# Kernel optimization log

Hardware: AMD Instinct MI355X
Metric: run time of the kernel (lower is better)

The kernel has to match this reference:

```python
import jax, jax.numpy as jnp
from jax import lax
import numpy as np

B, T, H, L = 4096, 7, 512, 256
D = 2 * H  # bidirectional LSTM feature dim


def _lstm(x, wih, whh, bih, bhh, reverse):
    # x: [B, T, L]; torch gate order i, f, g, o
    b, hdim = x.shape[0], whh.shape[0]
    xs = jnp.swapaxes(x, 0, 1)  # [T, B, L]
    bias = bih + bhh

    def step(carry, xt):
        h, c = carry
        gates = xt @ wih + h @ whh + bias
        i, f, g, o = jnp.split(gates, 4, axis=-1)
        c = jax.nn.sigmoid(f) * c + jax.nn.sigmoid(i) * jnp.tanh(g)
        h = jax.nn.sigmoid(o) * jnp.tanh(c)
        return (h, c), h

    h0 = jnp.zeros((b, hdim), x.dtype)
    _, hs = lax.scan(step, (h0, h0), xs, reverse=reverse)
    return jnp.swapaxes(hs, 0, 1)  # [B, T, H]


def _att(enc, dec):
    # Sequential attention: keys/values start as enc and grow with each decoder output.
    keys = enc  # [B, T, D]
    outs = []
    for i in range(dec.shape[1]):  # fixed small T=7, Python loop is static
        q = dec[:, i, :]                                  # [B, D]
        scores = jnp.einsum('bd,btd->bt', q, keys)        # dot over features
        a = jax.nn.softmax(scores, axis=1)
        ctx = jnp.einsum('bt,btd->bd', a, keys)
        out = ctx + q
        outs.append(out)
        keys = jnp.concatenate([keys, out[:, None, :]], axis=1)
    return jnp.stack(outs, axis=1)  # [B, T, D]


def _deconv(x, w, b):
    # torch ConvTranspose2d (stride 1, pad 0) == full conv with flipped, in/out-swapped kernel
    kh, kw = w.shape[2], w.shape[3]
    w2 = jnp.transpose(w[:, :, ::-1, ::-1], (1, 0, 2, 3))  # [out, in, kh, kw]
    y = lax.conv_general_dilated(x, w2, (1, 1), ((kh - 1, kh - 1), (kw - 1, kw - 1)),
                                 dimension_numbers=('NCHW', 'OIHW', 'NCHW'))
    return y + b[None, :, None, None]


def setup_inputs() -> dict:
    key = jax.random.key(0)
    ks = jax.random.split(key, 12)
    p = lambda k, shape: jax.random.normal(k, shape, jnp.float32) * 0.02
    return {
        'lstm_enc': jax.random.normal(ks[0], (B, T, D), jnp.float32),
        'gaussian_noise': jax.random.normal(ks[1], (B, L), jnp.float32),
        'embedrep_w': p(ks[2], (L, L * T)), 'embedrep_b': jnp.zeros((L * T,), jnp.float32),
        'wih_f': p(ks[3], (L, 4 * H)), 'whh_f': p(ks[4], (H, 4 * H)),
        'bih_f': jnp.zeros((4 * H,), jnp.float32), 'bhh_f': jnp.zeros((4 * H,), jnp.float32),
        'wih_b': p(ks[5], (L, 4 * H)), 'whh_b': p(ks[6], (H, 4 * H)),
        'bih_b': jnp.zeros((4 * H,), jnp.float32), 'bhh_b': jnp.zeros((4 * H,), jnp.float32),
        'emb_w': p(ks[7], (D, 1024)), 'emb_b': jnp.zeros((1024,), jnp.float32),
        'dc3_w': p(ks[8], (64, 32, 1, 3)), 'dc3_b': jnp.zeros((32,), jnp.float32),
        'dc1_w': p(ks[9], (32, 16, 1, 5)), 'dc1_b': jnp.zeros((16,), jnp.float32),
        'dc2_w': p(ks[10], (16, 1, 3, 3)), 'dc2_b': jnp.zeros((1,), jnp.float32),
        'infer': 0,
    }


def reference(lstm_enc, gaussian_noise, embedrep_w, embedrep_b,
              wih_f, whh_f, bih_f, bhh_f, wih_b, whh_b, bih_b, bhh_b,
              emb_w, emb_b, dc3_w, dc3_b, dc1_w, dc1_b, dc2_w, dc2_b, infer):
    b = lstm_enc.shape[0]
    g1 = jax.nn.soft_sign(gaussian_noise @ embedrep_w + embedrep_b)   # [B, L*T]
    rep = g1.reshape(b, T, L)                                          # [B, 7, L]
    hf = _lstm(rep, wih_f, whh_f, bih_f, bhh_f, False)
    hb = _lstm(rep, wih_b, whh_b, bih_b, bhh_b, True)
    lstm1 = jnp.concatenate([hf, hb], axis=-1)                         # [B, 7, 2H]
    att_out = _att(lstm_enc, lstm1)                                    # [B, 7, 2H]
    emb = att_out @ emb_w + emb_b                                      # [B, 7, 1024]
    up = jax.nn.soft_sign(emb).reshape(b * T, 64, 1, 16)
    x = jax.nn.leaky_relu(_deconv(up, dc3_w, dc3_b))                   # [B*7, 32, 1, 18]
    x = jax.nn.leaky_relu(_deconv(x, dc1_w, dc1_b))                    # [B*7, 16, 1, 22]
    x = jax.nn.leaky_relu(_deconv(x, dc2_w, dc2_b))                    # [B*7, 1, 3, 24]
    x = jax.nn.softmax(x, axis=2)                                      # softmax over H dim (=3)
    out = x.reshape(b, T, 1, 3, 24)[:, :, -1, :, :]                    # [B, 7, 3, 24]
    return out
```

## Files before the change

kernel.cpp:

```cpp
#include <hip/hip_runtime.h>
#include <stdint.h>


typedef __attribute__((ext_vector_type(4))) float f32x4;
typedef __attribute__((ext_vector_type(8))) short bf16x8;
typedef __attribute__((ext_vector_type(4))) unsigned short us4;

__device__ __forceinline__ unsigned short f2b(float f) {
  union { float f; unsigned u; } x; x.f = f;
  unsigned r = x.u + 0x7FFFu + ((x.u >> 16) & 1u);
  return (unsigned short)(r >> 16);
}
__device__ __forceinline__ float b2f(unsigned short s) {
  union { unsigned u; float f; } x; x.u = ((unsigned)s) << 16; return x.f;
}
__device__ __forceinline__ float sigmoidf(float x) {
  return 1.f / (1.f + __expf(-x));
}
__device__ __forceinline__ float fast_tanh(float x) {
  x = fminf(15.f, fmaxf(-15.f, x));
  float e = __expf(2.f * x);
  return (e - 1.f) / (e + 1.f);
}

__device__ __forceinline__ void gl_lds16(const void* g, void* l) {
  auto gp = reinterpret_cast<const __attribute__((address_space(1))) unsigned int*>(
      reinterpret_cast<uintptr_t>(g));
  auto lp = reinterpret_cast<__attribute__((address_space(3))) unsigned int*>(
      reinterpret_cast<uintptr_t>(l));
  __builtin_amdgcn_global_load_lds(gp, lp, 16, 0, 0);
}


__device__ __forceinline__ void stage256x32(const unsigned short* src, int ld,
                                            unsigned short* hbase, int tid) {
  const int row_in = tid >> 2;
  const int gidx = tid & 3;
#pragma unroll
  for (int r = 0; r < 4; ++r) {
    int row = r * 64 + row_in;
    int gsrc = gidx ^ ((row >> 1) & 3);
    gl_lds16(src + (size_t)row * ld + gsrc * 8, hbase + r * 2048 + (tid >> 6) * 512);
  }
}

__device__ __forceinline__ void stage128x32(const unsigned short* src, int ld,
                                            unsigned short* hbase, int tid) {
  const int row_in = tid >> 2;
  const int gidx = tid & 3;
#pragma unroll
  for (int r = 0; r < 2; ++r) {
    int row = r * 64 + row_in;
    int gsrc = gidx ^ ((row >> 1) & 3);
    gl_lds16(src + (size_t)row * ld + gsrc * 8, hbase + r * 2048 + (tid >> 6) * 512);
  }
}

__device__ __forceinline__ void stage128x32_t128(const unsigned short* src, int ld,
                                                 unsigned short* hbase, int tid) {
  const int row_in = tid >> 2;
  const int gidx = tid & 3;
#pragma unroll
  for (int r = 0; r < 4; ++r) {
    int row = r * 32 + row_in;
    int gsrc = gidx ^ ((row >> 1) & 3);
    gl_lds16(src + (size_t)row * ld + gsrc * 8, hbase + r * 1024 + (tid >> 6) * 512);
  }
}

__device__ __forceinline__ bf16x8 lds_fragH(const unsigned short* hbase, int row, int lq) {
  return *(const bf16x8*)(hbase + row * 32 + (lq ^ (((row >> 1) & 3) << 3)));
}

__device__ __forceinline__ void tile_w128(const unsigned short* Ab, const unsigned short* Bb,
                                          int wm, int wn, int lane, f32x4 (&acc)[8][4]) {
  const int lr = lane & 15, lq = (lane >> 4) * 8;
  bf16x8 b[4];
#pragma unroll
  for (int n = 0; n < 4; ++n) b[n] = lds_fragH(Bb, wn * 64 + n * 16 + lr, lq);
  bf16x8 a[8];
#pragma unroll
  for (int i = 0; i < 8; ++i) a[i] = lds_fragH(Ab, wm * 128 + i * 16 + lr, lq);
  __builtin_amdgcn_s_setprio(1);
#pragma unroll
  for (int i = 0; i < 8; ++i)
#pragma unroll
    for (int n = 0; n < 4; ++n)
      acc[i][n] = __builtin_amdgcn_mfma_f32_16x16x32_bf16(a[i], b[n], acc[i][n], 0, 0, 0);
  __builtin_amdgcn_s_setprio(0);
}

#define DBUF_SYNC()                                   \
  asm volatile("s_waitcnt vmcnt(0)" ::: "memory");    \
  __builtin_amdgcn_s_barrier();                       \
  __builtin_amdgcn_sched_barrier(0);

__device__ __forceinline__ void stage128x64(const unsigned short* src, int ld,
                                            unsigned short* lds, int wv, int lane) {
#pragma unroll
  for (int r = 0; r < 4; ++r) {
    int row = r * 32 + wv * 8 + (lane >> 3);
    gl_lds16(src + (size_t)row * ld + (lane & 7) * 8, lds + (r * 32 + wv * 8) * 64);
  }
}
__device__ __forceinline__ void mfma_tile(const unsigned short* As, const unsigned short* Bs,
                                          int wm, int wn, int lane, f32x4 acc[4][4]) {
#pragma unroll
  for (int kk = 0; kk < 2; ++kk) {
    int ko = kk * 32 + (lane >> 4) * 8;
    bf16x8 a[4], b[4];
#pragma unroll
    for (int i = 0; i < 4; ++i)
      a[i] = *(const bf16x8*)(As + (size_t)(wm * 64 + i * 16 + (lane & 15)) * 64 + ko);
#pragma unroll
    for (int i = 0; i < 4; ++i)
      b[i] = *(const bf16x8*)(Bs + (size_t)(wn * 64 + i * 16 + (lane & 15)) * 64 + ko);
#pragma unroll
    for (int mi = 0; mi < 4; ++mi)
#pragma unroll
      for (int ni = 0; ni < 4; ++ni)
        acc[mi][ni] = __builtin_amdgcn_mfma_f32_16x16x32_bf16(a[mi], b[ni], acc[mi][ni], 0, 0, 0);
  }
}

__global__ __launch_bounds__(256) void pack_kernel(
    const float* __restrict__ noise, const float* __restrict__ erep_w,
    const float* __restrict__ emb_w,
    const float* __restrict__ wih_f, const float* __restrict__ whh_f,
    const float* __restrict__ bih_f, const float* __restrict__ bhh_f,
    const float* __restrict__ wih_b, const float* __restrict__ whh_b,
    const float* __restrict__ bih_b, const float* __restrict__ bhh_b,
    unsigned short* __restrict__ noiseb, unsigned short* __restrict__ erepT,
    unsigned short* __restrict__ embT, unsigned short* __restrict__ lstmW,
    float* __restrict__ lstmB) {
  const int N0 = 4096 * 256 / 4;
  const int N1 = 1792 * 256 / 4;
  const int N2 = 1024 * 1024 / 4;
  const int N3 = 2 * 2048 * 768 / 4;
  const int N4 = 2 * 2048 / 4;
  const int total = N0 + N1 + N2 + N3 + N4;
  for (int i = blockIdx.x * 256 + threadIdx.x; i < total; i += gridDim.x * 256) {
    int x = i;
    if (x < N0) {
      f32x4 v = ((const f32x4*)noise)[x];
      us4 o4;
#pragma unroll
      for (int e = 0; e < 4; ++e) o4[e] = f2b(v[e]);
      ((us4*)noiseb)[x] = o4;
      continue;
    }
    x -= N0;
    if (x < N1) {
      int n = x >> 6, k4 = (x & 63) * 4;
      us4 o4;
#pragma unroll
      for (int e = 0; e < 4; ++e) o4[e] = f2b(erep_w[(size_t)(k4 + e) * 1792 + n]);
      ((us4*)erepT)[x] = o4;
      continue;
    }
    x -= N1;
    if (x < N2) {
      int n = x >> 8, k4 = (x & 255) * 4;
      int o = (n & 63) * 16 + (n >> 6);
      us4 o4;
#pragma unroll
      for (int e = 0; e < 4; ++e) o4[e] = f2b(emb_w[(size_t)(k4 + e) * 1024 + o]);
      ((us4*)embT)[x] = o4;
      continue;
    }
    x -= N2;
    if (x < N3) {
      int dir = x / (2048 * 192);
      int r = x - dir * (2048 * 192);
      int npk = r / 192, k4 = (r - npk * 192) * 4;
      int blk = npk >> 6, g = (npk >> 4) & 3, u = npk & 15;
      int o = g * 512 + blk * 16 + u;
      const float* wih = dir ? wih_b : wih_f;
      const float* whh = dir ? whh_b : whh_f;
      us4 o4;
#pragma unroll
      for (int e = 0; e < 4; ++e) {
        int k = k4 + e;
        float v = (k < 256) ? wih[(size_t)k * 2048 + o] : whh[(size_t)(k - 256) * 2048 + o];
        o4[e] = f2b(v);
      }
      ((us4*)lstmW)[x] = o4;
      continue;
    }
    x -= N3;
    {
      int dir = x >> 9, npk4 = (x & 511) * 4;
      int blk = npk4 >> 6, g = (npk4 >> 4) & 3, u = npk4 & 15;
      int o = g * 512 + blk * 16 + u;
      const float* bi = dir ? bih_b : bih_f;
      const float* bh = dir ? bhh_b : bhh_f;
      f32x4 o4;
#pragma unroll
      for (int e = 0; e < 4; ++e) o4[e] = bi[o + e] + bh[o + e];
      ((f32x4*)lstmB)[x] = o4;
    }
  }
}

__global__ __launch_bounds__(256) void gemm_rep_kernel(
    const unsigned short* __restrict__ A, const unsigned short* __restrict__ Bt,
    const float* __restrict__ bias, unsigned short* __restrict__ rep_t) {
  __shared__ unsigned short As[128 * 64];
  __shared__ unsigned short Bs[128 * 64];
  const int lane = threadIdx.x & 63, wv = threadIdx.x >> 6;
  const int wm = wv >> 1, wn = wv & 1;
  const int m0 = blockIdx.y * 128, n0 = blockIdx.x * 128;
  f32x4 acc[4][4];
#pragma unroll
  for (int i = 0; i < 4; ++i)
#pragma unroll
    for (int j = 0; j < 4; ++j) acc[i][j] = (f32x4){0.f, 0.f, 0.f, 0.f};
  for (int k0 = 0; k0 < 256; k0 += 64) {
    stage128x64(A + (size_t)m0 * 256 + k0, 256, As, wv, lane);
    stage128x64(Bt + (size_t)n0 * 256 + k0, 256, Bs, wv, lane);
    __syncthreads();
    mfma_tile(As, Bs, wm, wn, lane, acc);
    __syncthreads();
  }
#pragma unroll
  for (int ni = 0; ni < 4; ++ni) {
    int n = n0 + wn * 64 + ni * 16 + (lane & 15);
    float bv = bias[n];
    int t = n >> 8, l = n & 255;
#pragma unroll
    for (int mi = 0; mi < 4; ++mi)
#pragma unroll
      for (int r = 0; r < 4; ++r) {
        int m = m0 + wm * 64 + mi * 16 + (lane >> 4) * 4 + r;
        float v = acc[mi][ni][r] + bv;
        v = v / (1.f + fabsf(v));
        rep_t[((size_t)t * 4096 + m) * 256 + l] = f2b(v);
      }
  }
}

__global__ __launch_bounds__(128, 2) void lstm_step_kernel(
    const unsigned short* __restrict__ rep_t, const unsigned short* __restrict__ Wp,
    const float* __restrict__ biasP, unsigned short* __restrict__ hbuf,
    unsigned short* __restrict__ cbuf, unsigned short* __restrict__ lstm1, int step) {
  __shared__ unsigned short Ar[2][4096];
  __shared__ unsigned short Br[2][4096];
  const int tid = threadIdx.x, lane = tid & 63, wv = tid >> 6;
  const int swz = (blockIdx.x & 7) * 128 + (blockIdx.x >> 3);
  const int dir = swz >> 9;
  const int rem = swz & 511;
  const int by = rem >> 4, bx = rem & 15;
  const int m0 = by * 128, n0 = bx * 128;
  const int t_proc = dir ? (6 - step) : step;
  const unsigned short* W = Wp + (size_t)dir * 2048 * 768;
  const unsigned short* hin = hbuf + ((size_t)(step & 1) * 2 + dir) * (4096 * 512);
  unsigned short* hout = hbuf + ((size_t)((step + 1) & 1) * 2 + dir) * (4096 * 512);
  unsigned short* cp = cbuf + (size_t)dir * (4096 * 512);
  const unsigned short* xsrc = rep_t + (size_t)t_proc * 4096 * 256;

  f32x4 acc[8][4];
#pragma unroll
  for (int i = 0; i < 8; ++i)
#pragma unroll
    for (int j = 0; j < 4; ++j) acc[i][j] = (f32x4){0.f, 0.f, 0.f, 0.f};

  auto asrc = [&](int tt) {
    return tt < 8 ? xsrc + (size_t)m0 * 256 + tt * 32
                  : hin + (size_t)m0 * 512 + (tt - 8) * 32;
  };
  auto ald = [&](int tt) { return tt < 8 ? 256 : 512; };

  stage128x32_t128(asrc(0), ald(0), Ar[0], tid);
  stage128x32_t128(W + (size_t)n0 * 768 + 0 * 32, 768, Br[0], tid);
  DBUF_SYNC()

#pragma unroll
  for (int t = 0; t < 24; ++t) {
    if (t + 1 < 24) {
      stage128x32_t128(asrc(t + 1), ald(t + 1), Ar[(t + 1) & 1], tid);
      stage128x32_t128(W + (size_t)n0 * 768 + (t + 1) * 32, 768, Br[(t + 1) & 1], tid);
    }
    tile_w128(Ar[t & 1], Br[t & 1], 0, wv, lane, acc);
    if (t + 1 < 24) { DBUF_SYNC() }
  }

  const int u = lane & 15;
  const int blk = (n0 + wv * 64) >> 6;
  const int j = blk * 16 + u;
  const float bz0 = biasP[dir * 2048 + blk * 64 + 0 * 16 + u];
  const float bz1 = biasP[dir * 2048 + blk * 64 + 1 * 16 + u];
  const float bz2 = biasP[dir * 2048 + blk * 64 + 2 * 16 + u];
  const float bz3 = biasP[dir * 2048 + blk * 64 + 3 * 16 + u];
#pragma unroll
  for (int mi = 0; mi < 8; ++mi)
#pragma unroll
    for (int r = 0; r < 4; ++r) {
      int row = m0 + mi * 16 + (lane >> 4) * 4 + r;
      float gi = acc[mi][0][r] + bz0;
      float gf = acc[mi][1][r] + bz1;
      float gg = acc[mi][2][r] + bz2;
      float go = acc[mi][3][r] + bz3;
      size_t ci = (size_t)row * 512 + j;
      float c = sigmoidf(gf) * b2f(cp[ci]) + sigmoidf(gi) * fast_tanh(gg);
      cp[ci] = f2b(c);
      float h = sigmoidf(go) * fast_tanh(c);
      unsigned short hb = f2b(h);
      hout[ci] = hb;
      lstm1[((size_t)row * 7 + t_proc) * 1024 + dir * 512 + j] = hb;
    }
}

__global__ __launch_bounds__(256) void att_fused3_kernel(
    const float* __restrict__ enc, const unsigned short* __restrict__ lstm1,
    unsigned short* __restrict__ att) {
  __shared__ unsigned short Qs[7 * 1032];
  __shared__ unsigned short Es[7 * 1032];
  __shared__ float P[8 * 256];
  __shared__ float sG[98];
  __shared__ float sC[7][14];
  __shared__ float sA[16];
  const int tid = threadIdx.x, lane = tid & 63, wv = tid >> 6;
  const int b = blockIdx.x;
  const float* Eb = enc + (size_t)b * 7168;
  const unsigned short* Qb = lstm1 + (size_t)b * 7168;

  if (tid < 98) ((float*)sC)[tid] = 0.f;

  const f32x4* Eb4 = (const f32x4*)Eb;
  const int d0 = tid * 4;
#pragma unroll
  for (int r = 0; r < 7; ++r) {
    f32x4 v = Eb4[r * 256 + tid];
    us4 hi;
#pragma unroll
    for (int e = 0; e < 4; ++e) hi[e] = f2b(v[e]);
    *(us4*)&Es[r * 1032 + d0] = hi;
    *(us4*)&Qs[r * 1032 + d0] = *(const us4*)(Qb + r * 1024 + d0);
  }
  asm volatile("s_waitcnt lgkmcnt(0)" ::: "memory");
  __builtin_amdgcn_sched_barrier(0);

  {
    const int rr = lane & 15;
    const int rowc = rr % 7;
    const int kbase = wv * 256 + (lane >> 4) * 8;
    f32x4 g1 = {0.f, 0.f, 0.f, 0.f}, g2 = {0.f, 0.f, 0.f, 0.f};
#pragma unroll
    for (int s = 0; s < 8; ++s) {
      const int k0 = kbase + s * 32;
      bf16x8 aq = *(const bf16x8*)&Qs[rowc * 1032 + k0];
      bf16x8 be = *(const bf16x8*)&Es[rowc * 1032 + k0];
      g1 = __builtin_amdgcn_mfma_f32_16x16x32_bf16(aq, be, g1, 0, 0, 0);
      g2 = __builtin_amdgcn_mfma_f32_16x16x32_bf16(aq, aq, g2, 0, 0, 0);
    }
    *(f32x4*)&P[((wv * 2 + 0) * 64 + lane) * 4] = g1;
    *(f32x4*)&P[((wv * 2 + 1) * 64 + lane) * 4] = g2;
  }
  __syncthreads();

  if (tid < 98) {
    int i = tid / 14, v = tid - i * 14;
    int col = v < 7 ? v : v - 7;
    int tile = v < 7 ? 0 : 1;
    int ln = ((i >> 2) << 4) | col;
    int rg = i & 3;
    float s = 0.f;
#pragma unroll
    for (int w = 0; w < 4; ++w) s += P[((w * 2 + tile) * 64 + ln) * 4 + rg];
    sG[i * 14 + v] = s;
  }
  __syncthreads();
  if (wv == 0) {
    for (int i = 0; i < 7; ++i) {
      const int nt = 7 + i;
      float s = -1e30f;
      if (lane < 7) {
        s = sG[i * 14 + lane];
      } else if (lane < nt) {
        int jj = lane - 7;
        float a2 = 0.f;
#pragma unroll
        for (int v = 0; v < 14; ++v) a2 += sC[jj][v] * sG[i * 14 + v];
        s = a2;
      }
      float mx = s;
#pragma unroll
      for (int off = 8; off >= 1; off >>= 1) mx = fmaxf(mx, __shfl_xor(mx, off, 16));
      float e = (lane < nt) ? __expf(s - mx) : 0.f;
      float sum = e;
#pragma unroll
      for (int off = 8; off >= 1; off >>= 1) sum += __shfl_xor(sum, off, 16);
      float aw = e / sum;
      if (lane < 16) sA[lane] = aw;
      if (lane < 14) {
        float c = (lane < 7) ? sA[lane] : 0.f;
        for (int jj = 0; jj < i; ++jj) c += sA[7 + jj] * sC[jj][lane];
        if (lane == 7 + i) c += 1.f;
        sC[i][lane] = c;
      }
    }
  }
  __syncthreads();

  {
    float acc[7][4];
#pragma unroll
    for (int i = 0; i < 7; ++i)
#pragma unroll
      for (int e = 0; e < 4; ++e) acc[i][e] = 0.f;
#pragma unroll
    for (int t = 0; t < 7; ++t) {
      us4 ev = *(const us4*)&Es[t * 1032 + d0];
      float evf[4];
#pragma unroll
      for (int e = 0; e < 4; ++e) evf[e] = b2f(ev[e]);
#pragma unroll
      for (int i = 0; i < 7; ++i) {
        float c = sC[i][t];
#pragma unroll
        for (int e = 0; e < 4; ++e) acc[i][e] += c * evf[e];
      }
    }
#pragma unroll
    for (int m = 0; m < 7; ++m) {
      us4 qv = *(const us4*)&Qs[m * 1032 + d0];
      float qf[4];
#pragma unroll
      for (int e = 0; e < 4; ++e) qf[e] = b2f(qv[e]);
#pragma unroll
      for (int i = m; i < 7; ++i) {
        float c = sC[i][7 + m];
#pragma unroll
        for (int e = 0; e < 4; ++e) acc[i][e] += c * qf[e];
      }
    }
    unsigned short* Ab = att + (size_t)b * 7168;
#pragma unroll
    for (int i = 0; i < 7; ++i) {
      us4 r;
#pragma unroll
      for (int e = 0; e < 4; ++e) r[e] = f2b(acc[i][e]);
      *(us4*)(Ab + i * 1024 + d0) = r;
    }
  }
}

__global__ __launch_bounds__(256, 2) void gemm_emb_kernel(
    const unsigned short* __restrict__ A, const unsigned short* __restrict__ Bt,
    const float* __restrict__ bias, unsigned short* __restrict__ up_t) {
  __shared__ unsigned short Ar[2][8192];
  __shared__ unsigned short Br[2][4096];
  const int tid = threadIdx.x, lane = tid & 63, wv = tid >> 6;
  const int wm = wv >> 1, wn = wv & 1;
  const int swz = (blockIdx.x & 7) * 112 + (blockIdx.x >> 3);
  const int by = swz >> 3, bx = swz & 7;
  const int m0 = by * 256, n0 = bx * 128;

  f32x4 acc[8][4];
#pragma unroll
  for (int i = 0; i < 8; ++i)
#pragma unroll
    for (int j = 0; j < 4; ++j) acc[i][j] = (f32x4){0.f, 0.f, 0.f, 0.f};

  const unsigned short* Abase = A + (size_t)m0 * 1024;
  const unsigned short* Bbase = Bt + (size_t)n0 * 1024;

  stage256x32(Abase + 0 * 32, 1024, Ar[0], tid);
  stage128x32(Bbase + 0 * 32, 1024, Br[0], tid);
  DBUF_SYNC()

#pragma unroll
  for (int t = 0; t < 32; ++t) {
    if (t + 1 < 32) {
      stage256x32(Abase + (t + 1) * 32, 1024, Ar[(t + 1) & 1], tid);
      stage128x32(Bbase + (t + 1) * 32, 1024, Br[(t + 1) & 1], tid);
    }
    tile_w128(Ar[t & 1], Br[t & 1], wm, wn, lane, acc);
    if (t + 1 < 32) { DBUF_SYNC() }
  }

#pragma unroll
  for (int ni = 0; ni < 4; ++ni) {
    int np = n0 + wn * 64 + ni * 16 + (lane & 15);
    int o = (np & 63) * 16 + (np >> 6);
    float bv = bias[o];
#pragma unroll
    for (int mi = 0; mi < 8; ++mi)
#pragma unroll
      for (int r = 0; r < 4; ++r) {
        int m = m0 + wm * 128 + mi * 16 + (lane >> 4) * 4 + r;
        float v = acc[mi][ni][r] + bv;
        v = v / (1.f + fabsf(v));
        up_t[(size_t)m * 1024 + np] = f2b(v);
      }
  }
}

__global__ __launch_bounds__(256) void dc_fused_kernel(
    const unsigned short* __restrict__ up_t,
    const float* __restrict__ w3, const float* __restrict__ b3,
    const float* __restrict__ w1, const float* __restrict__ b1,
    const float* __restrict__ w2, const float* __restrict__ b2,
    float* __restrict__ out) {
  __shared__ unsigned short y1L[576 * 40];
  __shared__ unsigned short y2L[704 * 24];
  const int tid = threadIdx.x, lane = tid & 63, wv = tid >> 6;
  const int g0 = blockIdx.x * 32;
  const int kq = (lane >> 4) * 8;
  const int oc = lane & 15;

  {
    bf16x8 bf[2][6];
#pragma unroll
    for (int nt = 0; nt < 2; ++nt)
#pragma unroll
      for (int kk = 0; kk < 6; ++kk) {
        bf16x8 v;
#pragma unroll
        for (int t = 0; t < 8; ++t) {
          int k = kk * 32 + kq + t;
          int jj = k >> 6, ic = k & 63;
          v[t] = (short)f2b(w3[((size_t)ic * 32 + nt * 16 + oc) * 3 + jj]);
        }
        bf[nt][kk] = v;
      }
    const float bia0 = b3[oc], bia1 = b3[16 + oc];
    for (int c = wv; c < 36; c += 4) {
      int m = c * 16 + (lane & 15);
      int imgl = m / 18, ow = m - imgl * 18;
      const unsigned short* arow = up_t + (size_t)(g0 + imgl) * 1024;
      f32x4 acc0 = {0.f, 0.f, 0.f, 0.f}, acc1 = {0.f, 0.f, 0.f, 0.f};
#pragma unroll
      for (int kk = 0; kk < 6; ++kk) {
        int jj = kk >> 1;
        int ic0 = (kk & 1) * 32 + kq;
        int iw = ow - jj;
        bf16x8 a = {0, 0, 0, 0, 0, 0, 0, 0};
        if ((unsigned)iw < 16u) a = *(const bf16x8*)(arow + iw * 64 + ic0);
        acc0 = __builtin_amdgcn_mfma_f32_16x16x32_bf16(a, bf[0][kk], acc0, 0, 0, 0);
        acc1 = __builtin_amdgcn_mfma_f32_16x16x32_bf16(a, bf[1][kk], acc1, 0, 0, 0);
      }
#pragma unroll
      for (int r = 0; r < 4; ++r) {
        int mm = c * 16 + (lane >> 4) * 4 + r;
        float v0 = acc0[r] + bia0; v0 = v0 > 0.f ? v0 : 0.01f * v0;
        float v1 = acc1[r] + bia1; v1 = v1 > 0.f ? v1 : 0.01f * v1;
        y1L[mm * 40 + oc] = f2b(v0);
        y1L[mm * 40 + 16 + oc] = f2b(v1);
      }
    }
  }
  __syncthreads();

  {
    bf16x8 bf[5];
#pragma unroll
    for (int kk = 0; kk < 5; ++kk) {
      bf16x8 v;
#pragma unroll
      for (int t = 0; t < 8; ++t) {
        int ic = kq + t;
        v[t] = (short)f2b(w1[((size_t)ic * 16 + oc) * 5 + kk]);
      }
      bf[kk] = v;
    }
    const float bia = b1[oc];
    for (int c = wv; c < 44; c += 4) {
      int m = c * 16 + (lane & 15);
      int imgl = m / 22, ow = m - imgl * 22;
      const unsigned short* abase = y1L + imgl * (18 * 40);
      f32x4 acc = {0.f, 0.f, 0.f, 0.f};
#pragma unroll
      for (int kk = 0; kk < 5; ++kk) {
        int iw = ow - kk;
        bf16x8 a = {0, 0, 0, 0, 0, 0, 0, 0};
        if ((unsigned)iw < 18u) a = *(const bf16x8*)(abase + iw * 40 + kq);
        acc = __builtin_amdgcn_mfma_f32_16x16x32_bf16(a, bf[kk], acc, 0, 0, 0);
      }
#pragma unroll
      for (int r = 0; r < 4; ++r) {
        int mm = c * 16 + (lane >> 4) * 4 + r;
        float v = acc[r] + bia;
        v = v > 0.f ? v : 0.01f * v;
        y2L[mm * 24 + oc] = f2b(v);
      }
    }
  }
  __syncthreads();

  for (int ii = tid; ii < 768; ii += 256) {
    int imgl = ii / 24, ow = ii - imgl * 24;
    float lg0 = b2[0], lg1 = b2[0], lg2 = b2[0];
#pragma unroll
    for (int jj = 0; jj < 3; ++jj) {
      int iw = ow - jj;
      if ((unsigned)iw >= 22u) continue;
      const unsigned short* row = y2L + (imgl * 22 + iw) * 24;
      bf16x8 v0 = *(const bf16x8*)(row);
      bf16x8 v1 = *(const bf16x8*)(row + 8);
      float x[16];
#pragma unroll
      for (int ic = 0; ic < 8; ++ic) {
        x[ic] = b2f((unsigned short)v0[ic]);
        x[8 + ic] = b2f((unsigned short)v1[ic]);
      }
#pragma unroll
      for (int ic = 0; ic < 16; ++ic) {
        lg0 += x[ic] * w2[ic * 9 + 0 * 3 + jj];
        lg1 += x[ic] * w2[ic * 9 + 1 * 3 + jj];
        lg2 += x[ic] * w2[ic * 9 + 2 * 3 + jj];
      }
    }
    lg0 = lg0 > 0.f ? lg0 : 0.01f * lg0;
    lg1 = lg1 > 0.f ? lg1 : 0.01f * lg1;
    lg2 = lg2 > 0.f ? lg2 : 0.01f * lg2;
    float mx = fmaxf(lg0, fmaxf(lg1, lg2));
    float e0 = __expf(lg0 - mx), e1 = __expf(lg1 - mx), e2 = __expf(lg2 - mx);
    float inv = 1.f / (e0 + e1 + e2);
    size_t ob = (size_t)(g0 + imgl) * 72 + ow;
    out[ob] = e0 * inv;
    out[ob + 24] = e1 * inv;
    out[ob + 48] = e2 * inv;
  }
}

extern "C" void kernel_launch(void* const* d_in, const int* in_sizes, int n_in,
                              void* d_out, int out_size, void* d_ws, size_t ws_size,
                              hipStream_t stream) {
  (void)in_sizes; (void)n_in; (void)out_size; (void)ws_size;
  const float* enc    = (const float*)d_in[0];
  const float* noise  = (const float*)d_in[1];
  const float* erep_w = (const float*)d_in[2];
  const float* erep_b = (const float*)d_in[3];
  const float* wih_f  = (const float*)d_in[4];
  const float* whh_f  = (const float*)d_in[5];
  const float* bih_f  = (const float*)d_in[6];
  const float* bhh_f  = (const float*)d_in[7];
  const float* wih_b  = (const float*)d_in[8];
  const float* whh_b  = (const float*)d_in[9];
  const float* bih_b  = (const float*)d_in[10];
  const float* bhh_b  = (const float*)d_in[11];
  const float* emb_w  = (const float*)d_in[12];
  const float* emb_b  = (const float*)d_in[13];
  const float* dc3w   = (const float*)d_in[14];
  const float* dc3b   = (const float*)d_in[15];
  const float* dc1w   = (const float*)d_in[16];
  const float* dc1b   = (const float*)d_in[17];
  const float* dc2w   = (const float*)d_in[18];
  const float* dc2b   = (const float*)d_in[19];
  float* out = (float*)d_out;

  char* p = (char*)d_ws;
  auto carve = [&p](size_t bytes) {
    char* r = p;
    p += (bytes + 255) & ~(size_t)255;
    return r;
  };
  unsigned short* rep_t  = (unsigned short*)carve(7ull * 4096 * 256 * 2);
  unsigned short* lstmW  = (unsigned short*)carve(2ull * 2048 * 768 * 2);
  float*          lstmB  = (float*)carve(2ull * 2048 * 4);
  unsigned short* noiseb = (unsigned short*)carve(4096ull * 256 * 2);
  unsigned short* erepT  = (unsigned short*)carve(1792ull * 256 * 2);
  unsigned short* embT   = (unsigned short*)carve(1024ull * 1024 * 2);
  unsigned short* hbuf   = (unsigned short*)carve(4ull * 4096 * 512 * 2);
  unsigned short* cbuf   = (unsigned short*)carve(2ull * 4096 * 512 * 2);
  unsigned short* lstm1  = (unsigned short*)carve(4096ull * 7 * 1024 * 2);
  unsigned short* att    = (unsigned short*)carve(28672ull * 1024 * 2);
  unsigned short* up_t   = (unsigned short*)carve(28672ull * 1024 * 2);

  hipMemsetAsync(hbuf, 0, 2ull * 4096 * 512 * 2, stream);
  hipMemsetAsync(cbuf, 0, 2ull * 4096 * 512 * 2, stream);

  pack_kernel<<<2048, 256, 0, stream>>>(noise, erep_w, emb_w, wih_f, whh_f, bih_f, bhh_f,
                                        wih_b, whh_b, bih_b, bhh_b,
                                        noiseb, erepT, embT, lstmW, lstmB);
  gemm_rep_kernel<<<dim3(14, 32), 256, 0, stream>>>(noiseb, erepT, erep_b, rep_t);
  for (int s = 0; s < 7; ++s)
    lstm_step_kernel<<<1024, 128, 0, stream>>>(rep_t, lstmW, lstmB, hbuf, cbuf, lstm1, s);
  att_fused3_kernel<<<4096, 256, 0, stream>>>(enc, lstm1, att);
  gemm_emb_kernel<<<896, 256, 0, stream>>>(att, embT, emb_b, up_t);
  dc_fused_kernel<<<896, 256, 0, stream>>>(up_t, dc3w, dc3b, dc1w, dc1b, dc2w, dc2b, out);
}
```

Before: 523.2 us.

## Read LSTM hidden state from lstm1, skip zero h/c at step zero, enlarge tiles

The LSTM step kernel now reads the previous hidden state directly from the strided lstm1 output, which removes the separate h ping-pong buffer, its writes, and the memsets. The first step is specialised to run only the input-projection K-loop, skipping the h@Whh term and the old-c read because both are zero. Tiles grow from 128x128 with 2 waves to 256x128 with 4 waves to increase reuse of the weight tiles. The strided lstm1 reads (row stride 7168) may coalesce less well than the old contiguous h buffer, and the larger tiles halve the grid to 512 blocks.

```diff
diff --git a/kernel.cpp b/kernel.cpp
--- a/kernel.cpp
+++ b/kernel.cpp
@@ -53,18 +53,6 @@
     int row = r * 64 + row_in;
     int gsrc = gidx ^ ((row >> 1) & 3);
     gl_lds16(src + (size_t)row * ld + gsrc * 8, hbase + r * 2048 + (tid >> 6) * 512);
-  }
-}
-
-__device__ __forceinline__ void stage128x32_t128(const unsigned short* src, int ld,
-                                                 unsigned short* hbase, int tid) {
-  const int row_in = tid >> 2;
-  const int gidx = tid & 3;
-#pragma unroll
-  for (int r = 0; r < 4; ++r) {
-    int row = r * 32 + row_in;
-    int gsrc = gidx ^ ((row >> 1) & 3);
-    gl_lds16(src + (size_t)row * ld + gsrc * 8, hbase + r * 1024 + (tid >> 6) * 512);
   }
 }
 
@@ -239,24 +227,27 @@
   }
 }
 
-__global__ __launch_bounds__(128, 2) void lstm_step_kernel(
+template <int NT>
+__global__ __launch_bounds__(256, 2) void lstm_step_kernel(
     const unsigned short* __restrict__ rep_t, const unsigned short* __restrict__ Wp,
-    const float* __restrict__ biasP, unsigned short* __restrict__ hbuf,
-    unsigned short* __restrict__ cbuf, unsigned short* __restrict__ lstm1, int step) {
-  __shared__ unsigned short Ar[2][4096];
+    const float* __restrict__ biasP, unsigned short* __restrict__ cbuf,
+    unsigned short* __restrict__ lstm1, int step) {
+  __shared__ unsigned short Ar[2][8192];
   __shared__ unsigned short Br[2][4096];
   const int tid = threadIdx.x, lane = tid & 63, wv = tid >> 6;
-  const int swz = (blockIdx.x & 7) * 128 + (blockIdx.x >> 3);
-  const int dir = swz >> 9;
-  const int rem = swz & 511;
+  const int wm = wv >> 1, wn = wv & 1;
+  const int swz = (blockIdx.x & 7) * 64 + (blockIdx.x >> 3);
+  const int dir = swz >> 8;
+  const int rem = swz & 255;
   const int by = rem >> 4, bx = rem & 15;
-  const int m0 = by * 128, n0 = bx * 128;
+  const int m0 = by * 256, n0 = bx * 128;
   const int t_proc = dir ? (6 - step) : step;
+  const int t_prev = dir ? (t_proc + 1) : (t_proc - 1);
   const unsigned short* W = Wp + (size_t)dir * 2048 * 768;
-  const unsigned short* hin = hbuf + ((size_t)(step & 1) * 2 + dir) * (4096 * 512);
-  unsigned short* hout = hbuf + ((size_t)((step + 1) & 1) * 2 + dir) * (4096 * 512);
   unsigned short* cp = cbuf + (size_t)dir * (4096 * 512);
   const unsigned short* xsrc = rep_t + (size_t)t_proc * 4096 * 256;
+  const unsigned short* hsrc =
+      lstm1 + (size_t)((NT == 24) ? t_prev : 0) * 1024 + (size_t)dir * 512;
 
   f32x4 acc[8][4];
 #pragma unroll
@@ -266,26 +257,26 @@
 
   auto asrc = [&](int tt) {
     return tt < 8 ? xsrc + (size_t)m0 * 256 + tt * 32
-                  : hin + (size_t)m0 * 512 + (tt - 8) * 32;
+                  : hsrc + (size_t)m0 * 7168 + (tt - 8) * 32;
   };
-  auto ald = [&](int tt) { return tt < 8 ? 256 : 512; };
-
-  stage128x32_t128(asrc(0), ald(0), Ar[0], tid);
-  stage128x32_t128(W + (size_t)n0 * 768 + 0 * 32, 768, Br[0], tid);
+  auto ald = [&](int tt) { return tt < 8 ? 256 : 7168; };
+
+  stage256x32(asrc(0), ald(0), Ar[0], tid);
+  stage128x32(W + (size_t)n0 * 768 + 0 * 32, 768, Br[0], tid);
   DBUF_SYNC()
 
 #pragma unroll
-  for (int t = 0; t < 24; ++t) {
-    if (t + 1 < 24) {
-      stage128x32_t128(asrc(t + 1), ald(t + 1), Ar[(t + 1) & 1], tid);
-      stage128x32_t128(W + (size_t)n0 * 768 + (t + 1) * 32, 768, Br[(t + 1) & 1], tid);
-    }
-    tile_w128(Ar[t & 1], Br[t & 1], 0, wv, lane, acc);
-    if (t + 1 < 24) { DBUF_SYNC() }
+  for (int t = 0; t < NT; ++t) {
+    if (t + 1 < NT) {
+      stage256x32(asrc(t + 1), ald(t + 1), Ar[(t + 1) & 1], tid);
+      stage128x32(W + (size_t)n0 * 768 + (t + 1) * 32, 768, Br[(t + 1) & 1], tid);
+    }
+    tile_w128(Ar[t & 1], Br[t & 1], wm, wn, lane, acc);
+    if (t + 1 < NT) { DBUF_SYNC() }
   }
 
   const int u = lane & 15;
-  const int blk = (n0 + wv * 64) >> 6;
+  const int blk = (n0 + wn * 64) >> 6;
   const int j = blk * 16 + u;
   const float bz0 = biasP[dir * 2048 + blk * 64 + 0 * 16 + u];
   const float bz1 = biasP[dir * 2048 + blk * 64 + 1 * 16 + u];
@@ -295,18 +286,21 @@
   for (int mi = 0; mi < 8; ++mi)
 #pragma unroll
     for (int r = 0; r < 4; ++r) {
-      int row = m0 + mi * 16 + (lane >> 4) * 4 + r;
+      int row = m0 + wm * 128 + mi * 16 + (lane >> 4) * 4 + r;
       float gi = acc[mi][0][r] + bz0;
       float gf = acc[mi][1][r] + bz1;
       float gg = acc[mi][2][r] + bz2;
       float go = acc[mi][3][r] + bz3;
       size_t ci = (size_t)row * 512 + j;
-      float c = sigmoidf(gf) * b2f(cp[ci]) + sigmoidf(gi) * fast_tanh(gg);
+      float c;
+      if (NT == 8) {
+        c = sigmoidf(gi) * fast_tanh(gg);
+      } else {
+        c = sigmoidf(gf) * b2f(cp[ci]) + sigmoidf(gi) * fast_tanh(gg);
+      }
       cp[ci] = f2b(c);
       float h = sigmoidf(go) * fast_tanh(c);
-      unsigned short hb = f2b(h);
-      hout[ci] = hb;
-      lstm1[((size_t)row * 7 + t_proc) * 1024 + dir * 512 + j] = hb;
+      lstm1[((size_t)row * 7 + t_proc) * 1024 + dir * 512 + j] = f2b(h);
     }
 }
 
@@ -662,21 +656,18 @@
   unsigned short* noiseb = (unsigned short*)carve(4096ull * 256 * 2);
   unsigned short* erepT  = (unsigned short*)carve(1792ull * 256 * 2);
   unsigned short* embT   = (unsigned short*)carve(1024ull * 1024 * 2);
-  unsigned short* hbuf   = (unsigned short*)carve(4ull * 4096 * 512 * 2);
   unsigned short* cbuf   = (unsigned short*)carve(2ull * 4096 * 512 * 2);
   unsigned short* lstm1  = (unsigned short*)carve(4096ull * 7 * 1024 * 2);
   unsigned short* att    = (unsigned short*)carve(28672ull * 1024 * 2);
   unsigned short* up_t   = (unsigned short*)carve(28672ull * 1024 * 2);
 
-  hipMemsetAsync(hbuf, 0, 2ull * 4096 * 512 * 2, stream);
-  hipMemsetAsync(cbuf, 0, 2ull * 4096 * 512 * 2, stream);
-
   pack_kernel<<<2048, 256, 0, stream>>>(noise, erep_w, emb_w, wih_f, whh_f, bih_f, bhh_f,
                                         wih_b, whh_b, bih_b, bhh_b,
                                         noiseb, erepT, embT, lstmW, lstmB);
   gemm_rep_kernel<<<dim3(14, 32), 256, 0, stream>>>(noiseb, erepT, erep_b, rep_t);
-  for (int s = 0; s < 7; ++s)
-    lstm_step_kernel<<<1024, 128, 0, stream>>>(rep_t, lstmW, lstmB, hbuf, cbuf, lstm1, s);
+  lstm_step_kernel<8><<<512, 256, 0, stream>>>(rep_t, lstmW, lstmB, cbuf, lstm1, 0);
+  for (int s = 1; s < 7; ++s)
+    lstm_step_kernel<24><<<512, 256, 0, stream>>>(rep_t, lstmW, lstmB, cbuf, lstm1, s);
   att_fused3_kernel<<<4096, 256, 0, stream>>>(enc, lstm1, att);
   gemm_emb_kernel<<<896, 256, 0, stream>>>(att, embT, emb_b, up_t);
   dc_fused_kernel<<<896, 256, 0, stream>>>(up_t, dc3w, dc3b, dc1w, dc1b, dc2w, dc2b, out);
```

Result: faster. 468.7 us (-10.4%).
